# Kernel optimization log

Hardware: AMD Instinct MI355X
Metric: run time of the kernel (lower is better)

The kernel has to match this reference:

```python
import jax, jax.numpy as jnp
import numpy as np


def _conv3x3(x, w):
    # NCHW input, OIHW weight, stride 1, padding 1 (SAME for 3x3)
    return jax.lax.conv_general_dilated(
        x, w, window_strides=(1, 1), padding=((1, 1), (1, 1)),
        dimension_numbers=('NCHW', 'OIHW', 'NCHW'))


def _conv1x1(x, w):
    return jax.lax.conv_general_dilated(
        x, w, window_strides=(1, 1), padding=((0, 0), (0, 0)),
        dimension_numbers=('NCHW', 'OIHW', 'NCHW'))


def setup_inputs() -> dict:
    key = jax.random.key(0)
    k_x, k_w1, k_w2, k_wm = jax.random.split(key, 4)
    N, C, H, W = 16, 256, 64, 64
    fan = C * 9
    x = jax.random.normal(k_x, (N, C, H, W), dtype=jnp.float32)
    w1 = jax.random.normal(k_w1, (C, C, 3, 3), dtype=jnp.float32) * (2.0 / fan) ** 0.5
    w2 = jax.random.normal(k_w2, (C, C, 3, 3), dtype=jnp.float32) * (2.0 / fan) ** 0.5
    w_mask = jax.random.normal(k_wm, (1, C, 1, 1), dtype=jnp.float32) * (1.0 / C) ** 0.5
    b_mask = jnp.zeros((1,), dtype=jnp.float32)
    return {'x': x, 'w1': w1, 'w2': w2, 'w_mask': w_mask, 'b_mask': b_mask}


def reference(x, w1, w2, w_mask, b_mask):
    # MaskUnit: 1x1 conv -> logits -> hard binary mask (straight-through estimator)
    logits = _conv1x1(x, w_mask) + b_mask[None, :, None, None]  # [N,1,H,W]
    hard = (logits > 0).astype(x.dtype)
    mask = logits + jax.lax.stop_gradient(hard - logits)        # std mask, binary in fwd
    # dilated mask: 3x3 max-pool (covers 3x3 receptive field of active outputs)
    mask_dilate = jax.lax.reduce_window(
        mask, -jnp.inf, jax.lax.max, (1, 1, 3, 3), (1, 1, 1, 1), 'SAME')
    # sparse branch: conv1 gated by dilated mask, conv2 gated by std mask
    h = jax.nn.relu(_conv3x3(x, w1) * mask_dilate)
    h = jax.nn.relu(_conv3x3(h, w2) * mask)
    # apply_mask + residual (mask binary -> h*mask == h already, kept for fidelity)
    out = x + h * mask
    return out
```

## Files before the change

### kernel.cpp

```cpp
#include <hip/hip_runtime.h>
#include <hip/hip_bf16.h>

#define C_ 256
#define H_ 64
#define W_ 64
#define N_ 16
#define HW_ 4096
#define IMG_ (C_ * HW_)
#define PADIMG_ (66 * 66 * 256)
#define WT_ELEMS_ (9 * 256 * 256)

typedef short bf16x8 __attribute__((ext_vector_type(8)));
typedef float f32x4 __attribute__((ext_vector_type(4)));

__device__ __forceinline__ unsigned short f2bf(float f) {
  __hip_bfloat16 h = __float2bfloat16(f);
  return *reinterpret_cast<unsigned short*>(&h);
}

__device__ __forceinline__ void gld_lds16(const void* g, void* l) {
  __builtin_amdgcn_global_load_lds(
      (const __attribute__((address_space(1))) void*)g,
      (__attribute__((address_space(3))) void*)l, 16, 0, 0);
}

__global__ __launch_bounds__(256) void xpadmask_kernel(
    const float* __restrict__ x, const float* __restrict__ wm,
    const float* __restrict__ bm, short* __restrict__ Xp,
    unsigned char* __restrict__ mask) {
  __shared__ unsigned short lds[64 * 260];
  __shared__ float wms[256];
  __shared__ double sums[4][64];
  const int h = blockIdx.x, img = blockIdx.y;
  const int tid = threadIdx.x;
  const int wv = tid >> 6, wl = tid & 63;
  wms[tid] = wm[tid];
  __syncthreads();
  const float* xi = x + (size_t)img * IMG_ + h * 64;
  double a0 = 0.0, a1 = 0.0, a2 = 0.0, a3 = 0.0;
#pragma unroll 4
  for (int i = 0; i < 16; ++i) {
#pragma unroll
    for (int u = 0; u < 4; ++u) {
      int c = (i * 4 + u) * 4 + wv;
      float v = xi[(size_t)c * HW_ + wl];
      lds[wl * 260 + c] = f2bf(v);
      double p = (double)v * (double)wms[c];
      if (u == 0) a0 += p;
      else if (u == 1) a1 += p;
      else if (u == 2) a2 += p;
      else a3 += p;
    }
  }
  sums[wv][wl] = (a0 + a1) + (a2 + a3);
  __syncthreads();
  short* Xpi = Xp + (size_t)img * PADIMG_ + ((h + 1) * 66 + 1) * 256;
#pragma unroll
  for (int j = 0; j < 16; ++j) {
    int w = j * 4 + wv;
    int c4 = wl * 4;
    uint2 d = *(const uint2*)&lds[w * 260 + c4];
    *(uint2*)&Xpi[(size_t)w * 256 + c4] = d;
  }
  if (wv == 0) {
    double t = sums[0][wl] + sums[1][wl] + sums[2][wl] + sums[3][wl] +
               (double)bm[0];
    mask[img * HW_ + h * 64 + wl] = (t > 0.0) ? 1 : 0;
  }
}

__global__ __launch_bounds__(256) void dilate_kernel(
    const unsigned char* __restrict__ mask, unsigned char* __restrict__ md) {
  int pix = blockIdx.x * 256 + threadIdx.x;
  int n = pix >> 12;
  int hw = pix & (HW_ - 1);
  int h = hw >> 6, w = hw & 63;
  int m = 0;
  for (int dy = -1; dy <= 1; dy++) {
    int hh = h + dy;
    if (hh < 0 || hh >= H_) continue;
    for (int dx = -1; dx <= 1; dx++) {
      int ww = w + dx;
      if (ww < 0 || ww >= W_) continue;
      m |= mask[n * HW_ + hh * W_ + ww];
    }
  }
  md[pix] = (unsigned char)m;
}

__global__ __launch_bounds__(256) void wt_kernel(
    const float* __restrict__ w1, const float* __restrict__ w2,
    short* __restrict__ Wt1, short* __restrict__ Wt2) {
  const int k = blockIdx.x, c = threadIdx.x;
  const float* src = blockIdx.y ? w2 : w1;
  short* dst = blockIdx.y ? Wt2 : Wt1;
  const float* s = src + ((size_t)k * 256 + c) * 9;
#pragma unroll
  for (int t = 0; t < 9; ++t)
    dst[t * 65536 + k * 256 + c] = (short)f2bf(s[t]);
}

__global__ __launch_bounds__(128) void halo_zero(short* __restrict__ Xp,
                                                 short* __restrict__ Hp) {
  int p = blockIdx.x;
  int r, c;
  if (p < 66) { r = 0; c = p; }
  else if (p < 132) { r = 65; c = p - 66; }
  else if (p < 196) { r = p - 131; c = 0; }
  else { r = p - 195; c = 65; }
  short* buf = blockIdx.z ? Hp : Xp;
  unsigned int* d = (unsigned int*)(buf + (size_t)blockIdx.y * PADIMG_ +
                                    (size_t)(r * 66 + c) * 256);
  d[threadIdx.x] = 0u;
}

template <int EPI>
__global__ __launch_bounds__(256, 2) void conv_mfma(
    const short* __restrict__ src, const short* __restrict__ Wt,
    const unsigned char* __restrict__ gate, const float* __restrict__ xres,
    short* __restrict__ dstH, float* __restrict__ dstF) {
  __shared__ short Wl[3 * 64 * 32];
  __shared__ short Bl[672 * 32];

  const int tid = threadIdx.x;
  const int lane = tid & 63, wave = tid >> 6;
  const int quad = lane >> 4, ln15 = lane & 15;
  const int ch0 = blockIdx.x * 64;
  const int h0 = blockIdx.y * 8;
  const int img = blockIdx.z;

  const int lr = lane >> 2;
  const int lc = (lane & 3) * 8;

  const short* Xbase = src + (size_t)img * PADIMG_ + (size_t)(h0 * 66) * 256;
  const short* Wbase = Wt + (size_t)(ch0 + wave * 16 + lr) * 256 + lc;

  f32x4 acc[4][8];
#pragma unroll
  for (int i = 0; i < 4; ++i)
#pragma unroll
    for (int j = 0; j < 8; ++j) acc[i][j] = {0.f, 0.f, 0.f, 0.f};

  for (int kk = 0; kk < 8; ++kk) {
    const int ko = kk * 32;
    for (int n = wave; n < 42; n += 4) {
      gld_lds16(Xbase + (size_t)(n * 16 + lr) * 256 + ko + lc, Bl + n * 512);
    }
#pragma unroll
    for (int tl = 0; tl < 3; ++tl)
      gld_lds16(Wbase + (size_t)tl * 65536 + ko,
                Wl + (tl * 64 + wave * 16) * 32);
    __syncthreads();

#pragma unroll
    for (int dy = 0; dy < 3; ++dy) {
      bf16x8 a[4], b[8];
#pragma unroll
      for (int tl = 0; tl < 3; ++tl) {
#pragma unroll
        for (int i = 0; i < 4; ++i)
          a[i] = *(const bf16x8*)&Wl[(tl * 64 + i * 16 + ln15) * 32 + quad * 8];
#pragma unroll
        for (int j = 0; j < 8; ++j) {
          const int pl =
              (wave * 2 + (j >> 2) + dy) * 66 + (j & 3) * 16 + ln15 + tl;
          b[j] = *(const bf16x8*)&Bl[pl * 32 + quad * 8];
        }
#pragma unroll
        for (int i = 0; i < 4; ++i)
#pragma unroll
          for (int j = 0; j < 8; ++j)
            acc[i][j] = __builtin_amdgcn_mfma_f32_16x16x32_bf16(
                a[i], b[j], acc[i][j], 0, 0, 0);
      }
      __syncthreads();
      if (dy < 2) {
#pragma unroll
        for (int tl = 0; tl < 3; ++tl)
          gld_lds16(Wbase + (size_t)((dy + 1) * 3 + tl) * 65536 + ko,
                    Wl + (tl * 64 + wave * 16) * 32);
        __syncthreads();
      }
    }
  }

  const int rbase = h0 + wave * 2;
#pragma unroll
  for (int j = 0; j < 8; ++j) {
    const int r = rbase + (j >> 2);
    const int col = (j & 3) * 16 + ln15;
    const int pidx = r * 64 + col;
    const unsigned char g = gate[img * HW_ + pidx];
#pragma unroll
    for (int i = 0; i < 4; ++i) {
      f32x4 v = acc[i][j];
      const int ch = ch0 + i * 16 + quad * 4;
      float e0 = g ? fmaxf(v[0], 0.f) : 0.f;
      float e1 = g ? fmaxf(v[1], 0.f) : 0.f;
      float e2 = g ? fmaxf(v[2], 0.f) : 0.f;
      float e3 = g ? fmaxf(v[3], 0.f) : 0.f;
      if (EPI == 0) {
        uint2 u;
        u.x = (unsigned int)f2bf(e0) | ((unsigned int)f2bf(e1) << 16);
        u.y = (unsigned int)f2bf(e2) | ((unsigned int)f2bf(e3) << 16);
        short* d = dstH + (size_t)img * PADIMG_ +
                   ((size_t)((r + 1) * 66 + (col + 1))) * 256 + ch;
        *(uint2*)d = u;
      } else {
        size_t o = (size_t)img * IMG_ + (size_t)ch * HW_ + pidx;
        dstF[o] = xres[o] + e0;
        dstF[o + HW_] = xres[o + HW_] + e1;
        dstF[o + 2 * HW_] = xres[o + 2 * HW_] + e2;
        dstF[o + 3 * HW_] = xres[o + 3 * HW_] + e3;
      }
    }
  }
}

extern "C" void kernel_launch(void* const* d_in, const int* in_sizes, int n_in,
                              void* d_out, int out_size, void* d_ws,
                              size_t ws_size, hipStream_t stream) {
  const float* x = (const float*)d_in[0];
  const float* w1 = (const float*)d_in[1];
  const float* w2 = (const float*)d_in[2];
  const float* wmask = (const float*)d_in[3];
  const float* bmask = (const float*)d_in[4];
  float* out = (float*)d_out;

  char* ws = (char*)d_ws;
  unsigned char* mask = (unsigned char*)ws;
  unsigned char* md = (unsigned char*)(ws + 65536);
  short* Wt1 = (short*)(ws + 131072);
  short* Wt2 = Wt1 + WT_ELEMS_;
  short* Xp = (short*)(ws + 2490368);

  const size_t fixed = 2490368;
  const size_t tailpad = 32768;
  const size_t per_img = 2 * (size_t)PADIMG_ * 2;
  int B = (ws_size > fixed + tailpad)
              ? (int)((ws_size - fixed - tailpad) / per_img) : 0;
  if (B > N_) B = N_;
  if (B < 1) B = 1;
  short* Hp = Xp + (size_t)B * PADIMG_;

  wt_kernel<<<dim3(256, 2), 256, 0, stream>>>(w1, w2, Wt1, Wt2);
  halo_zero<<<dim3(260, B, 2), 128, 0, stream>>>(Xp, Hp);

  for (int n0 = 0; n0 < N_; n0 += B) {
    const int nb = (N_ - n0 < B) ? (N_ - n0) : B;
    xpadmask_kernel<<<dim3(64, nb), 256, 0, stream>>>(
        x + (size_t)n0 * IMG_, wmask, bmask, Xp, mask + n0 * HW_);
    dilate_kernel<<<nb * HW_ / 256, 256, 0, stream>>>(mask + n0 * HW_,
                                                      md + n0 * HW_);
    conv_mfma<0><<<dim3(4, 8, nb), 256, 0, stream>>>(
        Xp, Wt1, md + n0 * HW_, nullptr, Hp, nullptr);
    conv_mfma<1><<<dim3(4, 8, nb), 256, 0, stream>>>(
        Hp, Wt2, mask + n0 * HW_, x + (size_t)n0 * IMG_, nullptr,
        out + (size_t)n0 * IMG_);
  }
}
```

Before: 304.0 us.

## Double-buffer conv LDS tiles, switch to 32x32x16 MFMA, swizzle block order

Rewrites the conv main loop to stage all nine weight taps and the input tile for a 16-channel K slice into double-buffered LDS, so global loads for the next slice overlap with MFMA work on the current one. This replaces the per-dy barriers and weight reloads of the old loop. It also moves from 16x16x32 to 32x32x16 bf16 MFMA with a reorganised accumulator and epilogue, and adds a block-index swizzle that groups blocks sharing the same weight tile. In exchange it uses more LDS and larger accumulator vectors, which may limit occupancy.

Result: slower. 330.3 us (+8.7%).

```diff
diff --git a/kernel.cpp b/kernel.cpp
--- a/kernel.cpp
+++ b/kernel.cpp
@@ -11,7 +11,7 @@
 #define WT_ELEMS_ (9 * 256 * 256)
 
 typedef short bf16x8 __attribute__((ext_vector_type(8)));
-typedef float f32x4 __attribute__((ext_vector_type(4)));
+typedef float f32x16 __attribute__((ext_vector_type(16)));
 
 __device__ __forceinline__ unsigned short f2bf(float f) {
   __hip_bfloat16 h = __float2bfloat16(f);
@@ -114,104 +114,139 @@
   d[threadIdx.x] = 0u;
 }
 
+#define BREG 5280
+#define WBASE 21120
+#define WREG 4608
+
+__device__ __forceinline__ void stage_tile(short* sm, const short* Xb,
+                                           const short* Wt, int ch0, int buf,
+                                           int ko, int wave, int lane) {
+  short* Bd = sm + buf * 2 * BREG;
+  short* Wd = sm + WBASE + buf * 2 * WREG;
+#pragma unroll
+  for (int q = 0; q < 6; ++q) {
+    int n = wave + 4 * q;
+    if (n > 21) n = 21;
+    const int h = (n >= 11) ? 1 : 0;
+    const int i = n - h * 11;
+    const int row0 = (i < 10) ? i * 64 : 596;
+    gld_lds16(Xb + (size_t)(row0 + lane) * 256 + ko + h * 8,
+              Bd + h * BREG + row0 * 8);
+  }
+#pragma unroll
+  for (int q = 0; q < 5; ++q) {
+    int n = wave + 4 * q;
+    if (n > 17) n = 17;
+    const int h = (n >= 9) ? 1 : 0;
+    const int t = n - h * 9;
+    gld_lds16(Wt + (size_t)t * 65536 + (size_t)(ch0 + lane) * 256 + ko + h * 8,
+              Wd + h * WREG + t * 512);
+  }
+}
+
 template <int EPI>
 __global__ __launch_bounds__(256, 2) void conv_mfma(
     const short* __restrict__ src, const short* __restrict__ Wt,
     const unsigned char* __restrict__ gate, const float* __restrict__ xres,
-    short* __restrict__ dstH, float* __restrict__ dstF) {
-  __shared__ short Wl[3 * 64 * 32];
-  __shared__ short Bl[672 * 32];
+    short* __restrict__ dstH, float* __restrict__ dstF, int swz) {
+  __shared__ __align__(16) short sm[39552];
 
   const int tid = threadIdx.x;
   const int lane = tid & 63, wave = tid >> 6;
-  const int quad = lane >> 4, ln15 = lane & 15;
-  const int ch0 = blockIdx.x * 64;
-  const int h0 = blockIdx.y * 8;
-  const int img = blockIdx.z;
-
-  const int lr = lane >> 2;
-  const int lc = (lane & 3) * 8;
-
-  const short* Xbase = src + (size_t)img * PADIMG_ + (size_t)(h0 * 66) * 256;
-  const short* Wbase = Wt + (size_t)(ch0 + wave * 16 + lr) * 256 + lc;
-
-  f32x4 acc[4][8];
-#pragma unroll
-  for (int i = 0; i < 4; ++i)
-#pragma unroll
-    for (int j = 0; j < 8; ++j) acc[i][j] = {0.f, 0.f, 0.f, 0.f};
-
-  for (int kk = 0; kk < 8; ++kk) {
-    const int ko = kk * 32;
-    for (int n = wave; n < 42; n += 4) {
-      gld_lds16(Xbase + (size_t)(n * 16 + lr) * 256 + ko + lc, Bl + n * 512);
-    }
-#pragma unroll
-    for (int tl = 0; tl < 3; ++tl)
-      gld_lds16(Wbase + (size_t)tl * 65536 + ko,
-                Wl + (tl * 64 + wave * 16) * 32);
-    __syncthreads();
-
-#pragma unroll
-    for (int dy = 0; dy < 3; ++dy) {
-      bf16x8 a[4], b[8];
-#pragma unroll
-      for (int tl = 0; tl < 3; ++tl) {
-#pragma unroll
-        for (int i = 0; i < 4; ++i)
-          a[i] = *(const bf16x8*)&Wl[(tl * 64 + i * 16 + ln15) * 32 + quad * 8];
-#pragma unroll
-        for (int j = 0; j < 8; ++j) {
-          const int pl =
-              (wave * 2 + (j >> 2) + dy) * 66 + (j & 3) * 16 + ln15 + tl;
-          b[j] = *(const bf16x8*)&Bl[pl * 32 + quad * 8];
-        }
-#pragma unroll
-        for (int i = 0; i < 4; ++i)
-#pragma unroll
-          for (int j = 0; j < 8; ++j)
-            acc[i][j] = __builtin_amdgcn_mfma_f32_16x16x32_bf16(
-                a[i], b[j], acc[i][j], 0, 0, 0);
+  const int ln31 = lane & 31, kh = lane >> 5;
+
+  int bx, by, bz;
+  {
+    int d = blockIdx.x + 4 * (blockIdx.y + 8 * blockIdx.z);
+    if (swz) {
+      int k = d & 7, j = d >> 3;
+      bx = j & 3;
+      by = (j >> 2) & 7;
+      bz = ((j >> 5) << 3) + k;
+    } else {
+      bx = blockIdx.x;
+      by = blockIdx.y;
+      bz = blockIdx.z;
+    }
+  }
+  const int ch0 = bx * 64;
+  const int h0 = by * 8;
+  const int img = bz;
+
+  const short* Xb = src + (size_t)img * PADIMG_ + (size_t)(h0 * 66) * 256;
+
+  f32x16 acc[2][4];
+#pragma unroll
+  for (int i = 0; i < 2; ++i)
+#pragma unroll
+    for (int j = 0; j < 4; ++j)
+#pragma unroll
+      for (int e = 0; e < 16; ++e) acc[i][j][e] = 0.f;
+
+  stage_tile(sm, Xb, Wt, ch0, 0, 0, wave, lane);
+  asm volatile("s_waitcnt vmcnt(0)\n\ts_barrier" ::: "memory");
+
+#pragma unroll 2
+  for (int kk = 0; kk < 16; ++kk) {
+    const int cur = kk & 1;
+    if (kk < 15) stage_tile(sm, Xb, Wt, ch0, cur ^ 1, (kk + 1) * 16, wave, lane);
+
+    const short* Bth = sm + (cur * 2 + kh) * BREG + (wave * 132 + ln31) * 8;
+    const short* Wth = sm + WBASE + (cur * 2 + kh) * WREG + ln31 * 8;
+#pragma unroll
+    for (int t = 0; t < 9; ++t) {
+      const int dy = t / 3, dx = t % 3;
+      bf16x8 a0 = *(const bf16x8*)(Wth + t * 512);
+      bf16x8 a1 = *(const bf16x8*)(Wth + t * 512 + 256);
+      bf16x8 b[4];
+#pragma unroll
+      for (int j = 0; j < 4; ++j) {
+        const int off = (((j >> 1) + dy) * 66 + (j & 1) * 32 + dx) * 8;
+        b[j] = *(const bf16x8*)(Bth + off);
       }
-      __syncthreads();
-      if (dy < 2) {
-#pragma unroll
-        for (int tl = 0; tl < 3; ++tl)
-          gld_lds16(Wbase + (size_t)((dy + 1) * 3 + tl) * 65536 + ko,
-                    Wl + (tl * 64 + wave * 16) * 32);
-        __syncthreads();
+#pragma unroll
+      for (int j = 0; j < 4; ++j) {
+        acc[0][j] = __builtin_amdgcn_mfma_f32_32x32x16_bf16(a0, b[j],
+                                                            acc[0][j], 0, 0, 0);
+        acc[1][j] = __builtin_amdgcn_mfma_f32_32x32x16_bf16(a1, b[j],
+                                                            acc[1][j], 0, 0, 0);
       }
     }
-  }
-
-  const int rbase = h0 + wave * 2;
-#pragma unroll
-  for (int j = 0; j < 8; ++j) {
-    const int r = rbase + (j >> 2);
-    const int col = (j & 3) * 16 + ln15;
+    if (kk < 15)
+      asm volatile("s_waitcnt vmcnt(0)\n\ts_barrier" ::: "memory");
+  }
+
+  const int rb = h0 + wave * 2;
+#pragma unroll
+  for (int j = 0; j < 4; ++j) {
+    const int r = rb + (j >> 1);
+    const int col = (j & 1) * 32 + ln31;
     const int pidx = r * 64 + col;
     const unsigned char g = gate[img * HW_ + pidx];
 #pragma unroll
-    for (int i = 0; i < 4; ++i) {
-      f32x4 v = acc[i][j];
-      const int ch = ch0 + i * 16 + quad * 4;
-      float e0 = g ? fmaxf(v[0], 0.f) : 0.f;
-      float e1 = g ? fmaxf(v[1], 0.f) : 0.f;
-      float e2 = g ? fmaxf(v[2], 0.f) : 0.f;
-      float e3 = g ? fmaxf(v[3], 0.f) : 0.f;
-      if (EPI == 0) {
-        uint2 u;
-        u.x = (unsigned int)f2bf(e0) | ((unsigned int)f2bf(e1) << 16);
-        u.y = (unsigned int)f2bf(e2) | ((unsigned int)f2bf(e3) << 16);
-        short* d = dstH + (size_t)img * PADIMG_ +
-                   ((size_t)((r + 1) * 66 + (col + 1))) * 256 + ch;
-        *(uint2*)d = u;
-      } else {
-        size_t o = (size_t)img * IMG_ + (size_t)ch * HW_ + pidx;
-        dstF[o] = xres[o] + e0;
-        dstF[o + HW_] = xres[o + HW_] + e1;
-        dstF[o + 2 * HW_] = xres[o + 2 * HW_] + e2;
-        dstF[o + 3 * HW_] = xres[o + 3 * HW_] + e3;
+    for (int i = 0; i < 2; ++i) {
+      const f32x16 v = acc[i][j];
+#pragma unroll
+      for (int rg = 0; rg < 4; ++rg) {
+        const int ch = ch0 + i * 32 + rg * 8 + kh * 4;
+        float e0 = g ? fmaxf(v[rg * 4 + 0], 0.f) : 0.f;
+        float e1 = g ? fmaxf(v[rg * 4 + 1], 0.f) : 0.f;
+        float e2 = g ? fmaxf(v[rg * 4 + 2], 0.f) : 0.f;
+        float e3 = g ? fmaxf(v[rg * 4 + 3], 0.f) : 0.f;
+        if (EPI == 0) {
+          uint2 u;
+          u.x = (unsigned int)f2bf(e0) | ((unsigned int)f2bf(e1) << 16);
+          u.y = (unsigned int)f2bf(e2) | ((unsigned int)f2bf(e3) << 16);
+          short* dp = dstH + (size_t)img * PADIMG_ +
+                      ((size_t)((r + 1) * 66 + (col + 1))) * 256 + ch;
+          *(uint2*)dp = u;
+        } else {
+          size_t o = (size_t)img * IMG_ + (size_t)ch * HW_ + pidx;
+          dstF[o] = xres[o] + e0;
+          dstF[o + HW_] = xres[o + HW_] + e1;
+          dstF[o + 2 * HW_] = xres[o + 2 * HW_] + e2;
+          dstF[o + 3 * HW_] = xres[o + 3 * HW_] + e3;
+        }
       }
     }
   }
@@ -248,14 +283,15 @@
 
   for (int n0 = 0; n0 < N_; n0 += B) {
     const int nb = (N_ - n0 < B) ? (N_ - n0) : B;
+    const int swz = (nb % 8 == 0) ? 1 : 0;
     xpadmask_kernel<<<dim3(64, nb), 256, 0, stream>>>(
         x + (size_t)n0 * IMG_, wmask, bmask, Xp, mask + n0 * HW_);
     dilate_kernel<<<nb * HW_ / 256, 256, 0, stream>>>(mask + n0 * HW_,
                                                       md + n0 * HW_);
     conv_mfma<0><<<dim3(4, 8, nb), 256, 0, stream>>>(
-        Xp, Wt1, md + n0 * HW_, nullptr, Hp, nullptr);
+        Xp, Wt1, md + n0 * HW_, nullptr, Hp, nullptr, swz);
     conv_mfma<1><<<dim3(4, 8, nb), 256, 0, stream>>>(
         Hp, Wt2, mask + n0 * HW_, x + (size_t)n0 * IMG_, nullptr,
-        out + (size_t)n0 * IMG_);
-  }
-}
+        out + (size_t)n0 * IMG_, swz);
+  }
+}
```
